# Kernel optimization log

Hardware: AMD Instinct MI355X
Metric: run time of the kernel (lower is better)

The kernel has to match this reference:

```python
import jax, jax.numpy as jnp
import numpy as np

DIM = 1024
HEADS = 16
HEAD_DIM = DIM // HEADS
SCALE = HEAD_DIM ** -0.5


def setup_inputs() -> dict:
    key = jax.random.key(0)
    ks = jax.random.split(key, 6)
    B, N, C = 2, 2048, DIM
    s = C ** -0.5
    return {
        "x": jax.random.normal(ks[0], (B, N, C), dtype=jnp.float32),
        "Wq": jax.random.normal(ks[1], (C, C), dtype=jnp.float32) * s,
        "Wk": jax.random.normal(ks[2], (C, C), dtype=jnp.float32) * s,
        "Wv": jax.random.normal(ks[3], (C, C), dtype=jnp.float32) * s,
        "Wo": jax.random.normal(ks[4], (C, C), dtype=jnp.float32) * s,
        "bo": jax.random.normal(ks[5], (C,), dtype=jnp.float32) * 0.02,
    }


def reference(x, Wq, Wk, Wv, Wo, bo):
    B, N, C = x.shape
    H, D = HEADS, HEAD_DIM
    # q/k/v linears (no bias), reshape to [B, H, N, D]
    q = (x @ Wq.T).reshape(B, N, H, D).transpose(0, 2, 1, 3)
    k = (x @ Wk.T).reshape(B, N, H, D).transpose(0, 2, 1, 3)
    v = (x @ Wv.T).reshape(B, N, H, D).transpose(0, 2, 1, 3)
    attn = jnp.einsum("bhnd,bhmd->bhnm", q, k) * SCALE  # [B,H,N,N]
    attn = jax.nn.softmax(attn, axis=-1)
    out = jnp.einsum("bhnm,bhmd->bhnd", attn, v)  # [B,H,N,D]
    out = out.transpose(0, 2, 1, 3).reshape(B, N, C)
    out = out @ Wo.T + bo  # proj (dropout p=0 in eval -> identity)
    return out
```

## Files before the change

kernel.cpp:

```cpp
#include <hip/hip_runtime.h>
#include <stdint.h>

typedef __attribute__((ext_vector_type(8))) _Float16 half8;
typedef __attribute__((ext_vector_type(8))) unsigned short ushort8;
typedef __attribute__((ext_vector_type(4))) float f32x4;
typedef unsigned short u16;

#define AS1C(p) ((const __attribute__((address_space(1))) void*)(p))
#define AS3(p)  ((__attribute__((address_space(3))) void*)(p))

#define PIPE_W4 do { asm volatile("s_waitcnt vmcnt(4)" ::: "memory"); \
  __builtin_amdgcn_s_barrier(); __builtin_amdgcn_sched_barrier(0); } while (0)
#define PIPE_W0 do { asm volatile("s_waitcnt vmcnt(0)" ::: "memory"); \
  __builtin_amdgcn_s_barrier(); __builtin_amdgcn_sched_barrier(0); } while (0)

__device__ __forceinline__ f32x4 mfma_k32(half8 a, half8 b, f32x4 c) {
  return __builtin_amdgcn_mfma_f32_16x16x32_f16(a, b, c, 0, 0, 0);
}
__device__ __forceinline__ u16 f2h(float f) {
  return __builtin_bit_cast(u16, (_Float16)f);
}
__device__ __forceinline__ float fexp2(float x) {
  return __builtin_amdgcn_exp2f(x);
}
__device__ __forceinline__ unsigned int pk2h(float a, float b) {
  return __builtin_bit_cast(unsigned int, __builtin_amdgcn_cvt_pkrtz(a, b));
}
__device__ __forceinline__ int fsz(int r) {
  return (((r & 3) | (((r >> 3) & 1) << 2)) << 4);
}

__global__ __launch_bounds__(256) void k_convert(
    const float* __restrict__ x, const float* __restrict__ wq,
    const float* __restrict__ wk, const float* __restrict__ wv,
    const float* __restrict__ wo,
    u16* __restrict__ xb, u16* __restrict__ wqkvb, u16* __restrict__ wob) {
  size_t t = (size_t)blockIdx.x * 256 + threadIdx.x;
  size_t e = t * 8;
  const float* src;
  u16* dst;
  if (e < 4194304u)      { src = x  + e;            dst = xb    + e; }
  else if (e < 5242880u) { src = wq + (e-4194304u); dst = wqkvb + (e-4194304u); }
  else if (e < 6291456u) { src = wk + (e-5242880u); dst = wqkvb + (e-4194304u); }
  else if (e < 7340032u) { src = wv + (e-6291456u); dst = wqkvb + (e-4194304u); }
  else                   { src = wo + (e-7340032u); dst = wob   + (e-7340032u); }
  float4 a = *(const float4*)src;
  float4 b = *(const float4*)(src + 4);
  ushort8 o;
  o[0]=f2h(a.x); o[1]=f2h(a.y); o[2]=f2h(a.z); o[3]=f2h(a.w);
  o[4]=f2h(b.x); o[5]=f2h(b.y); o[6]=f2h(b.z); o[7]=f2h(b.w);
  *(ushort8*)dst = o;
}

__device__ __forceinline__ void gemm_core(
    const u16* __restrict__ Ag, const u16* __restrict__ Bg,
    int row0, int col0, char* lAc, char* lBc, f32x4 acc[4][4]) {
  const int tid = threadIdx.x;
  const int w = tid >> 6, lane = tid & 63;
  const int wm = (w >> 1) * 64, wn = (w & 1) * 64;
  const int l15 = lane & 15, l4 = lane >> 4;
#pragma unroll
  for (int i = 0; i < 4; ++i)
#pragma unroll
    for (int j = 0; j < 4; ++j) acc[i][j] = (f32x4){0.f, 0.f, 0.f, 0.f};

  const int lrow = lane >> 2;
  const int lcb  = (lane & 3) << 4;
  const char* Abase = (const char*)Ag + (size_t)row0 * 2048;
  const char* Bbase = (const char*)Bg + (size_t)col0 * 2048;

  auto stage = [&](int buf, int kt) {
#pragma unroll
    for (int i = 0; i < 2; ++i) {
      int c = w + 4 * i;
      int r = c * 16 + lrow;
      __builtin_amdgcn_global_load_lds(AS1C(Abase + (size_t)r * 2048 + kt * 64 + lcb),
                                       AS3(lAc + buf * 8192 + c * 1024), 16, 0, 0);
      __builtin_amdgcn_global_load_lds(AS1C(Bbase + (size_t)r * 2048 + kt * 64 + lcb),
                                       AS3(lBc + buf * 8192 + c * 1024), 16, 0, 0);
    }
  };
  auto compute = [&](int buf) {
    const char* A = lAc + buf * 8192;
    const char* B = lBc + buf * 8192;
    half8 af[4], bf[4];
#pragma unroll
    for (int mi = 0; mi < 4; ++mi)
      af[mi] = *(const half8*)(A + (wm + mi * 16 + l15) * 64 + (l4 << 4));
#pragma unroll
    for (int ni = 0; ni < 4; ++ni)
      bf[ni] = *(const half8*)(B + (wn + ni * 16 + l15) * 64 + (l4 << 4));
#pragma unroll
    for (int mi = 0; mi < 4; ++mi)
#pragma unroll
      for (int ni = 0; ni < 4; ++ni)
        acc[mi][ni] = mfma_k32(af[mi], bf[ni], acc[mi][ni]);
  };

  stage(0, 0);
  stage(1, 1);
  for (int k3 = 0; k3 < 30; k3 += 3) {
    PIPE_W4; stage(2, k3 + 2); compute(0);
    PIPE_W4; stage(0, k3 + 3); compute(1);
    PIPE_W4; stage(1, k3 + 4); compute(2);
  }
  PIPE_W4; compute(0);
  PIPE_W0; compute(1);
}

__global__ __launch_bounds__(256) void k_gemm_qkv(
    const u16* __restrict__ xb, const u16* __restrict__ wqkvb,
    u16* __restrict__ qk, u16* __restrict__ vt) {
  __shared__ u16 lA[3 * 4096];
  __shared__ u16 lB[3 * 4096];
  f32x4 acc[4][4];
  const int lid = blockIdx.x;
  const int xcd = lid & 7, idx = lid >> 3;
  const int pr = idx / 12, pc = idx % 12;
  const int row0 = (((xcd & 3) << 3) + pr) << 7;
  const int col0 = ((xcd >> 2) * 12 + pc) << 7;
  gemm_core(xb, wqkvb, row0, col0, (char*)lA, (char*)lB, acc);

  const int w = threadIdx.x >> 6, lane = threadIdx.x & 63;
  const int l15 = lane & 15, l4 = lane >> 4;
  const int rbase = row0 + (w >> 1) * 64 + (l4 << 2);
  const int cbase = col0 + (w & 1) * 64 + l15;
  const bool isQ = (col0 < 1024);
  const bool isV = (col0 >= 2048);
#pragma unroll
  for (int mi = 0; mi < 4; ++mi) {
#pragma unroll
    for (int ni = 0; ni < 4; ++ni) {
      const int col = cbase + ni * 16;
      if (!isV) {
#pragma unroll
        for (int r = 0; r < 4; ++r) {
          int row = rbase + mi * 16 + r;
          float v = acc[mi][ni][r];
          if (isQ) v *= 0.18033688f;
          qk[(size_t)row * 2048 + col] = f2h(v);
        }
      } else {
        const int jj = col - 2048;
        const int h = jj >> 6, d = jj & 63;
        const int row = rbase + mi * 16;
        const int b = row >> 11, n = row & 2047;
        u16 pk[4];
#pragma unroll
        for (int r = 0; r < 4; ++r) pk[r] = f2h(acc[mi][ni][r]);
        *(uint2*)&vt[(size_t)(((b << 4) + h) * 64 + d) * 2048 + n] = *(uint2*)pk;
      }
    }
  }
}

__global__ __launch_bounds__(256) void k_attn(
    const u16* __restrict__ qk, const u16* __restrict__ vt, u16* __restrict__ ao) {
  __shared__ u16 KV[6][4096];
  char* L = (char*)&KV[0][0];
  const int lid = blockIdx.x;
  const int xcd = lid & 7, sub = lid >> 3;
  const int bh = (xcd << 2) + (sub >> 5);
  const int qt = sub & 31;
  const int b = bh >> 4, h = bh & 15;
  const int w = threadIdx.x >> 6, lane = threadIdx.x & 63;
  const int l15 = lane & 15, l4 = lane >> 4;

  const int qrow = (b << 11) + (qt << 6) + (w << 4) + l15;
  half8 qf[2];
  qf[0] = *(const half8*)(qk + (size_t)qrow * 2048 + h * 64 + (l4 << 3));
  qf[1] = *(const half8*)(qk + (size_t)qrow * 2048 + h * 64 + 32 + (l4 << 3));

  half8 vones8;
#pragma unroll
  for (int j = 0; j < 8; ++j) vones8[j] = (_Float16)1.0f;

  const int lrow = lane >> 3;
  const int lcb  = (lane & 7) << 4;
  const char* Kbase = (const char*)qk + (size_t)(b << 11) * 4096 + 2048 + h * 128;
  const char* Vbase = (const char*)vt + (size_t)(bh * 64) * 4096;

  const int rr0 = (w << 3) + lrow;
  const int sc0 = lcb ^ fsz(rr0);
  const char* kg0 = Kbase + (size_t)rr0 * 4096 + sc0;
  const char* kg1 = kg0 + 131072;
  const char* vg0 = Vbase + (size_t)rr0 * 4096 + sc0;
  const char* vg1 = vg0 + 131072;
  const int kd0 = w * 1024, kd1 = (w + 4) * 1024;

  const int keybase = ((l15 >> 2) << 3) + (l15 & 3);
  const int kswz = fsz(keybase);
  const int vswz = (((l15 & 3) | (((l15 >> 3) & 1) << 2)) << 4);
  int koff[8], voff[8];
#pragma unroll
  for (int nt = 0; nt < 4; ++nt) {
    const int key = keybase + ((nt & 1) << 2) + ((nt >> 1) << 5);
    koff[2 * nt]     = key * 128 + ((l4 << 4) ^ kswz);
    koff[2 * nt + 1] = key * 128 + (((l4 << 4) + 64) ^ kswz);
  }
#pragma unroll
  for (int dt = 0; dt < 4; ++dt) {
    const int d = dt * 16 + l15;
    voff[2 * dt]     = 24576 + d * 128 + ((l4 << 4) ^ vswz);
    voff[2 * dt + 1] = 24576 + d * 128 + (((l4 << 4) + 64) ^ vswz);
  }

  float m_run = -1e30f;
  f32x4 acc_o[4];
  f32x4 acc_l = (f32x4){0.f, 0.f, 0.f, 0.f};
#pragma unroll
  for (int dt = 0; dt < 4; ++dt) acc_o[dt] = (f32x4){0.f, 0.f, 0.f, 0.f};

  auto stage = [&](int buf) {
    __builtin_amdgcn_global_load_lds(AS1C(kg0), AS3(L + buf * 8192 + kd0), 16, 0, 0);
    __builtin_amdgcn_global_load_lds(AS1C(kg1), AS3(L + buf * 8192 + kd1), 16, 0, 0);
    __builtin_amdgcn_global_load_lds(AS1C(vg0), AS3(L + 24576 + buf * 8192 + kd0), 16, 0, 0);
    __builtin_amdgcn_global_load_lds(AS1C(vg1), AS3(L + 24576 + buf * 8192 + kd1), 16, 0, 0);
    kg0 += 262144; kg1 += 262144; vg0 += 128; vg1 += 128;
  };

  auto compute = [&](int bu) {
    const char* Lb = L + bu * 8192;

    f32x4 s[4];
    __builtin_amdgcn_s_setprio(1);
#pragma unroll
    for (int nt = 0; nt < 4; ++nt) {
      half8 k0 = *(const half8*)(Lb + koff[2 * nt]);
      half8 k1 = *(const half8*)(Lb + koff[2 * nt + 1]);
      f32x4 z = (f32x4){0.f, 0.f, 0.f, 0.f};
      z = mfma_k32(k0, qf[0], z);
      s[nt] = mfma_k32(k1, qf[1], z);
    }
    __builtin_amdgcn_s_setprio(0);

    float t0 = fmaxf(fmaxf(s[0][0], s[0][1]), s[0][2]);
    float t1 = fmaxf(fmaxf(s[0][3], s[1][0]), s[1][1]);
    float t2 = fmaxf(fmaxf(s[1][2], s[1][3]), s[2][0]);
    float t3 = fmaxf(fmaxf(s[2][1], s[2][2]), s[2][3]);
    float t4 = fmaxf(fmaxf(s[3][0], s[3][1]), s[3][2]);
    float tm = fmaxf(fmaxf(fmaxf(t0, t1), fmaxf(t2, t3)), fmaxf(t4, s[3][3]));

    const bool skip = __all(tm - m_run <= 8.f);
    float mnew = m_run;
    if (!skip) {
      tm = fmaxf(tm, __shfl_xor(tm, 16));
      tm = fmaxf(tm, __shfl_xor(tm, 32));
      mnew = fmaxf(m_run, tm);
      float alpha = fexp2(m_run - mnew);
      m_run = mnew;
#pragma unroll
      for (int dt = 0; dt < 4; ++dt)
#pragma unroll
        for (int r = 0; r < 4; ++r) acc_o[dt][r] *= alpha;
      acc_l[0] *= alpha;
    }

    half8 pb[2];
#pragma unroll
    for (int p = 0; p < 2; ++p) {
      uint4 pk;
      pk.x = pk2h(fexp2(s[2*p][0] - mnew),   fexp2(s[2*p][1] - mnew));
      pk.y = pk2h(fexp2(s[2*p][2] - mnew),   fexp2(s[2*p][3] - mnew));
      pk.z = pk2h(fexp2(s[2*p+1][0] - mnew), fexp2(s[2*p+1][1] - mnew));
      pk.w = pk2h(fexp2(s[2*p+1][2] - mnew), fexp2(s[2*p+1][3] - mnew));
      pb[p] = __builtin_bit_cast(half8, pk);
    }

    __builtin_amdgcn_s_setprio(1);
#pragma unroll
    for (int dt = 0; dt < 4; ++dt) {
      half8 v0 = *(const half8*)(Lb + voff[2 * dt]);
      half8 v1 = *(const half8*)(Lb + voff[2 * dt + 1]);
      acc_o[dt] = mfma_k32(v0, pb[0], acc_o[dt]);
      acc_o[dt] = mfma_k32(v1, pb[1], acc_o[dt]);
    }
    acc_l = mfma_k32(vones8, pb[0], acc_l);
    acc_l = mfma_k32(vones8, pb[1], acc_l);
    __builtin_amdgcn_s_setprio(0);
  };

  stage(0);
  stage(1);
  for (int k3 = 0; k3 < 30; k3 += 3) {
    PIPE_W4; stage(2); compute(0);
    PIPE_W4; stage(0); compute(1);
    PIPE_W4; stage(1); compute(2);
  }
  PIPE_W4; compute(0);
  PIPE_W0; compute(1);

  const float inv = __builtin_amdgcn_rcpf(acc_l[0]);
  const size_t rowbase = ((size_t)(b << 11) + (qt << 6) + (w << 4) + l15) * 1024 + h * 64;
#pragma unroll
  for (int dt = 0; dt < 4; ++dt) {
    uint2 o;
    o.x = pk2h(acc_o[dt][0] * inv, acc_o[dt][1] * inv);
    o.y = pk2h(acc_o[dt][2] * inv, acc_o[dt][3] * inv);
    *(uint2*)&ao[rowbase + dt * 16 + (l4 << 2)] = o;
  }
}

__global__ __launch_bounds__(256) void k_gemm_proj(
    const u16* __restrict__ aob, const u16* __restrict__ wob,
    const float* __restrict__ bo, float* __restrict__ out) {
  __shared__ u16 lA[3 * 4096];
  __shared__ u16 lB[3 * 4096];
  f32x4 acc[4][4];
  const int lid = blockIdx.x;
  const int xcd = lid & 7, idx = lid >> 3;
  const int row0 = ((xcd << 2) + (idx >> 3)) << 7;
  const int col0 = (idx & 7) << 7;
  gemm_core(aob, wob, row0, col0, (char*)lA, (char*)lB, acc);

  const int w = threadIdx.x >> 6, lane = threadIdx.x & 63;
  const int l15 = lane & 15, l4 = lane >> 4;
  const int rbase = row0 + (w >> 1) * 64 + (l4 << 2);
  const int cbase = col0 + (w & 1) * 64 + l15;
#pragma unroll
  for (int mi = 0; mi < 4; ++mi) {
#pragma unroll
    for (int ni = 0; ni < 4; ++ni) {
      const int col = cbase + ni * 16;
      const float bb = bo[col];
#pragma unroll
      for (int r = 0; r < 4; ++r) {
        const int row = rbase + mi * 16 + r;
        out[(size_t)row * 1024 + col] = acc[mi][ni][r] + bb;
      }
    }
  }
}

extern "C" void kernel_launch(void* const* d_in, const int* in_sizes, int n_in,
                              void* d_out, int out_size, void* d_ws, size_t ws_size,
                              hipStream_t stream) {
  const float* x  = (const float*)d_in[0];
  const float* wq = (const float*)d_in[1];
  const float* wk = (const float*)d_in[2];
  const float* wv = (const float*)d_in[3];
  const float* wo = (const float*)d_in[4];
  const float* bo = (const float*)d_in[5];
  float* out = (float*)d_out;

  char* ws = (char*)d_ws;
  u16* xb    = (u16*)(ws);
  u16* wqkvb = (u16*)(ws + 8388608);
  u16* wob   = (u16*)(ws + 14680064);
  u16* qkb   = (u16*)(ws + 16777216);
  u16* vtb   = (u16*)(ws + 33554432);
  u16* aob   = (u16*)(ws + 41943040);

  k_convert<<<dim3(4096), dim3(256), 0, stream>>>(x, wq, wk, wv, wo, xb, wqkvb, wob);
  k_gemm_qkv<<<dim3(768), dim3(256), 0, stream>>>(xb, wqkvb, qkb, vtb);
  k_attn<<<dim3(1024), dim3(256), 0, stream>>>(qkb, vtb, aob);
  k_gemm_proj<<<dim3(256), dim3(256), 0, stream>>>(aob, wob, bo, out);
}
```

Before: 124.9 us.

## Double attention block to 8 waves and 128 query rows sharing each KV tile

The attention kernel now runs 512 threads (8 waves) per block over 128 query rows instead of 64, on half as many blocks. Each KV tile staged into LDS is reused by twice as many query rows, and each thread issues one K and one V async load per stage instead of two each, with the vmcnt wait lowered to match. This halves global KV traffic per query row. In exchange there are fewer blocks (512 for the device's CUs) and barriers now span 8 waves, which may hurt latency hiding and occupancy.

After: 115.8 us. -7.3%, faster.

```diff
diff --git a/kernel.cpp b/kernel.cpp
--- a/kernel.cpp
+++ b/kernel.cpp
@@ -9,9 +9,7 @@
 #define AS1C(p) ((const __attribute__((address_space(1))) void*)(p))
 #define AS3(p)  ((__attribute__((address_space(3))) void*)(p))
 
-#define PIPE_W4 do { asm volatile("s_waitcnt vmcnt(4)" ::: "memory"); \
-  __builtin_amdgcn_s_barrier(); __builtin_amdgcn_sched_barrier(0); } while (0)
-#define PIPE_W0 do { asm volatile("s_waitcnt vmcnt(0)" ::: "memory"); \
+#define PIPE_WAIT(n) do { asm volatile("s_waitcnt vmcnt(" #n ")" ::: "memory"); \
   __builtin_amdgcn_s_barrier(); __builtin_amdgcn_sched_barrier(0); } while (0)
 
 __device__ __forceinline__ f32x4 mfma_k32(half8 a, half8 b, f32x4 c) {
@@ -100,12 +98,12 @@
   stage(0, 0);
   stage(1, 1);
   for (int k3 = 0; k3 < 30; k3 += 3) {
-    PIPE_W4; stage(2, k3 + 2); compute(0);
-    PIPE_W4; stage(0, k3 + 3); compute(1);
-    PIPE_W4; stage(1, k3 + 4); compute(2);
-  }
-  PIPE_W4; compute(0);
-  PIPE_W0; compute(1);
+    PIPE_WAIT(4); stage(2, k3 + 2); compute(0);
+    PIPE_WAIT(4); stage(0, k3 + 3); compute(1);
+    PIPE_WAIT(4); stage(1, k3 + 4); compute(2);
+  }
+  PIPE_WAIT(4); compute(0);
+  PIPE_WAIT(0); compute(1);
 }
 
 __global__ __launch_bounds__(256) void k_gemm_qkv(
@@ -154,19 +152,19 @@
   }
 }
 
-__global__ __launch_bounds__(256) void k_attn(
+__global__ __launch_bounds__(512) void k_attn(
     const u16* __restrict__ qk, const u16* __restrict__ vt, u16* __restrict__ ao) {
   __shared__ u16 KV[6][4096];
   char* L = (char*)&KV[0][0];
   const int lid = blockIdx.x;
   const int xcd = lid & 7, sub = lid >> 3;
-  const int bh = (xcd << 2) + (sub >> 5);
-  const int qt = sub & 31;
+  const int bh = (xcd << 2) + (sub >> 4);
+  const int qt = sub & 15;
   const int b = bh >> 4, h = bh & 15;
   const int w = threadIdx.x >> 6, lane = threadIdx.x & 63;
   const int l15 = lane & 15, l4 = lane >> 4;
 
-  const int qrow = (b << 11) + (qt << 6) + (w << 4) + l15;
+  const int qrow = (b << 11) + (qt << 7) + (w << 4) + l15;
   half8 qf[2];
   qf[0] = *(const half8*)(qk + (size_t)qrow * 2048 + h * 64 + (l4 << 3));
   qf[1] = *(const half8*)(qk + (size_t)qrow * 2048 + h * 64 + 32 + (l4 << 3));
@@ -183,10 +181,8 @@
   const int rr0 = (w << 3) + lrow;
   const int sc0 = lcb ^ fsz(rr0);
   const char* kg0 = Kbase + (size_t)rr0 * 4096 + sc0;
-  const char* kg1 = kg0 + 131072;
   const char* vg0 = Vbase + (size_t)rr0 * 4096 + sc0;
-  const char* vg1 = vg0 + 131072;
-  const int kd0 = w * 1024, kd1 = (w + 4) * 1024;
+  const int kd0 = w * 1024;
 
   const int keybase = ((l15 >> 2) << 3) + (l15 & 3);
   const int kswz = fsz(keybase);
@@ -213,10 +209,8 @@
 
   auto stage = [&](int buf) {
     __builtin_amdgcn_global_load_lds(AS1C(kg0), AS3(L + buf * 8192 + kd0), 16, 0, 0);
-    __builtin_amdgcn_global_load_lds(AS1C(kg1), AS3(L + buf * 8192 + kd1), 16, 0, 0);
     __builtin_amdgcn_global_load_lds(AS1C(vg0), AS3(L + 24576 + buf * 8192 + kd0), 16, 0, 0);
-    __builtin_amdgcn_global_load_lds(AS1C(vg1), AS3(L + 24576 + buf * 8192 + kd1), 16, 0, 0);
-    kg0 += 262144; kg1 += 262144; vg0 += 128; vg1 += 128;
+    kg0 += 262144; vg0 += 128;
   };
 
   auto compute = [&](int bu) {
@@ -283,15 +277,15 @@
   stage(0);
   stage(1);
   for (int k3 = 0; k3 < 30; k3 += 3) {
-    PIPE_W4; stage(2); compute(0);
-    PIPE_W4; stage(0); compute(1);
-    PIPE_W4; stage(1); compute(2);
-  }
-  PIPE_W4; compute(0);
-  PIPE_W0; compute(1);
+    PIPE_WAIT(2); stage(2); compute(0);
+    PIPE_WAIT(2); stage(0); compute(1);
+    PIPE_WAIT(2); stage(1); compute(2);
+  }
+  PIPE_WAIT(2); compute(0);
+  PIPE_WAIT(0); compute(1);
 
   const float inv = __builtin_amdgcn_rcpf(acc_l[0]);
-  const size_t rowbase = ((size_t)(b << 11) + (qt << 6) + (w << 4) + l15) * 1024 + h * 64;
+  const size_t rowbase = ((size_t)(b << 11) + (qt << 7) + (w << 4) + l15) * 1024 + h * 64;
 #pragma unroll
   for (int dt = 0; dt < 4; ++dt) {
     uint2 o;
@@ -353,6 +347,6 @@
 
   k_convert<<<dim3(4096), dim3(256), 0, stream>>>(x, wq, wk, wv, wo, xb, wqkvb, wob);
   k_gemm_qkv<<<dim3(768), dim3(256), 0, stream>>>(xb, wqkvb, qkb, vtb);
-  k_attn<<<dim3(1024), dim3(256), 0, stream>>>(qkb, vtb, aob);
+  k_attn<<<dim3(512), dim3(512), 0, stream>>>(qkb, vtb, aob);
   k_gemm_proj<<<dim3(256), dim3(256), 0, stream>>>(aob, wob, bo, out);
 }
```
